# Kernel tuning notes

Hardware: AMD Instinct MI355X
Metric: run time of the kernel (lower is better)

The kernel has to match this reference:

```python
import jax, jax.numpy as jnp
import numpy as np

N_NODES = 100000
N_EDGES = 1600000
IN_CH = 128
OUT_CH = 128


def setup_inputs() -> dict:
    key = jax.random.key(0)
    k1, k2, k3 = jax.random.split(key, 3)
    x = jax.random.normal(k1, (N_NODES, IN_CH), dtype=jnp.float32)
    edge_index = jax.random.randint(k2, (2, N_EDGES), 0, N_NODES, dtype=jnp.int64)
    # Glorot-style init like PyG GCNConv
    W = jax.random.normal(k3, (IN_CH, OUT_CH), dtype=jnp.float32) * (1.0 / np.sqrt(IN_CH))
    b = jnp.zeros((OUT_CH,), dtype=jnp.float32)
    return {"x": x, "edge_index": edge_index, "W": W, "b": b}


def reference(x, edge_index, W, b):
    N = x.shape[0]
    # add self-loops (PyG GCNConv default add_self_loops=True)
    loop = jnp.arange(N, dtype=edge_index.dtype)
    src = jnp.concatenate([edge_index[0], loop])
    dst = jnp.concatenate([edge_index[1], loop])
    # symmetric normalization: deg computed over destination (col)
    deg = jax.ops.segment_sum(jnp.ones_like(src, dtype=x.dtype), dst, num_segments=N)
    dinv = jnp.where(deg > 0, jax.lax.rsqrt(deg), 0.0)
    norm = dinv[src] * dinv[dst]  # [E+N]
    xw = x @ W  # [N, out_ch]
    msg = xw[src] * norm[:, None]  # gather + scale, [E+N, out_ch]
    out = jax.ops.segment_sum(msg, dst, num_segments=N) + b  # scatter-add
    return jax.nn.relu(out)
```

## Files before the change

### kernel.cpp

```cpp
#include <hip/hip_runtime.h>
#include <hip/hip_bf16.h>

constexpr int CH    = 128;
constexpr int BSH   = 7;
constexpr int CAPSH = 12;
constexpr int CHUNK = 3125;
constexpr int CHCAP = 3200;
constexpr int BKCAP = 2816;

typedef __attribute__((ext_vector_type(8))) short short8v;
typedef __attribute__((ext_vector_type(4))) float f32x4;

__device__ __forceinline__ unsigned short f2bf(float f) {
    unsigned u = __float_as_uint(f);
    u = (u + 0x7fffu + ((u >> 16) & 1u)) >> 16;
    return (unsigned short)u;
}

__global__ __launch_bounds__(256) void k_bin(const int* __restrict__ src,
                                             const int* __restrict__ dst, int E,
                                             int* __restrict__ bucket_cnt,
                                             unsigned* __restrict__ packed,
                                             const float* __restrict__ W,
                                             unsigned short* __restrict__ Wt) {
    __shared__ int hist[1024];
    __shared__ int start[1024];
    __shared__ int cursor[1024];
    __shared__ int gofs[1024];
    __shared__ int tscan[256];
    __shared__ unsigned       sorted[CHCAP];
    __shared__ unsigned short sbkt[CHCAP];

    int t = threadIdx.x;
    if (blockIdx.x < 32) {
        int idx = blockIdx.x * 256 + t;
        int c  = idx & 127;
        int k2 = (idx >> 7) * 2;
        unsigned pk = (unsigned)f2bf(W[(size_t)k2 * CH + c]) |
                      ((unsigned)f2bf(W[(size_t)(k2 + 1) * CH + c]) << 16);
        *(unsigned*)(Wt + (size_t)c * CH + k2) = pk;
    }
    #pragma unroll
    for (int i = 0; i < 4; ++i) hist[t + i * 256] = 0;
    __syncthreads();

    int e0 = blockIdx.x * CHUNK;
    int e1 = min(e0 + CHUNK, E);
    for (int e = e0 + t; e < e1; e += 256)
        atomicAdd(&hist[dst[e] >> BSH], 1);
    __syncthreads();
    int b4 = t * 4;
    int c0 = hist[b4], c1 = hist[b4 + 1], c2 = hist[b4 + 2], c3 = hist[b4 + 3];
    int tsum = c0 + c1 + c2 + c3;
    tscan[t] = tsum;
    __syncthreads();
    for (int off = 1; off < 256; off <<= 1) {
        int v = (t >= off) ? tscan[t - off] : 0;
        __syncthreads();
        tscan[t] += v;
        __syncthreads();
    }
    int eb = tscan[t] - tsum;
    start[b4]     = eb;
    start[b4 + 1] = eb + c0;
    start[b4 + 2] = eb + c0 + c1;
    start[b4 + 3] = eb + c0 + c1 + c2;
    cursor[b4]     = eb;
    cursor[b4 + 1] = eb + c0;
    cursor[b4 + 2] = eb + c0 + c1;
    cursor[b4 + 3] = eb + c0 + c1 + c2;
    __syncthreads();
    #pragma unroll
    for (int i = 0; i < 4; ++i) {
        int b = t + i * 256;
        int c = hist[b];
        gofs[b] = (c > 0) ? atomicAdd(&bucket_cnt[b], c) : 0;
    }
    __syncthreads();
    for (int e = e0 + t; e < e1; e += 256) {
        int d = dst[e];
        int b = d >> BSH;
        int pos = atomicAdd(&cursor[b], 1);
        sorted[pos] = (unsigned)src[e] | ((unsigned)(d & ((1 << BSH) - 1)) << 20);
        sbkt[pos] = (unsigned short)b;
    }
    __syncthreads();
    int nloc = e1 - e0;
    for (int i = t; i < nloc; i += 256) {
        int b = sbkt[i];
        int gpos = (b << CAPSH) + gofs[b] + (i - start[b]);
        packed[gpos] = sorted[i];
    }
}

__global__ __launch_bounds__(256) void k_deg(const int* __restrict__ bucket_cnt,
                                             const unsigned* __restrict__ packed,
                                             float* __restrict__ dinv, int N) {
    __shared__ int fh[128];
    int b = blockIdx.x;
    int t = threadIdx.x;
    int cnt = bucket_cnt[b];
    if (t < 128) fh[t] = 0;
    __syncthreads();
    const unsigned* pk = packed + ((size_t)b << CAPSH);
    for (int i = t; i < cnt; i += 256)
        atomicAdd(&fh[(pk[i] >> 20) & 127], 1);
    __syncthreads();
    if (t < 128) {
        int node = (b << BSH) + t;
        if (node < N) dinv[node] = rsqrtf((float)fh[t] + 1.0f);
    }
}

__global__ __launch_bounds__(256) void k_gemm(const float* __restrict__ x,
                                              const unsigned short* __restrict__ Wt,
                                              const float* __restrict__ dinv,
                                              unsigned short* __restrict__ xwb, int N) {
    __shared__ __align__(16) unsigned short xs[64 * CH];
    int t = threadIdx.x;
    int w = t >> 6, lane = t & 63;
    int c16 = lane & 15, kq = lane >> 4, kb = kq * 8;
    int row0 = blockIdx.x * 64;
    int arow = row0 + w * 16 + c16;
    bool av = arow < N;
    const float* xp = x + (size_t)(av ? arow : 0) * CH;

    f32x4 acc[8];
    #pragma unroll
    for (int f = 0; f < 8; ++f) acc[f] = (f32x4){0.f, 0.f, 0.f, 0.f};

    #pragma unroll
    for (int kc = 0; kc < 4; ++kc) {
        float4 x0 = make_float4(0.f, 0.f, 0.f, 0.f), x1 = x0;
        if (av) {
            x0 = ((const float4*)(xp + kc * 32 + kb))[0];
            x1 = ((const float4*)(xp + kc * 32 + kb))[1];
        }
        union { short8v v; __hip_bfloat162 h[4]; } au;
        au.h[0] = __float22bfloat162_rn(make_float2(x0.x, x0.y));
        au.h[1] = __float22bfloat162_rn(make_float2(x0.z, x0.w));
        au.h[2] = __float22bfloat162_rn(make_float2(x1.x, x1.y));
        au.h[3] = __float22bfloat162_rn(make_float2(x1.z, x1.w));
        #pragma unroll
        for (int f = 0; f < 8; ++f) {
            short8v b = *(const short8v*)(Wt + (size_t)(f * 16 + c16) * CH + kc * 32 + kb);
            acc[f] = __builtin_amdgcn_mfma_f32_16x16x32_bf16(au.v, b, acc[f], 0, 0, 0);
        }
    }

    #pragma unroll
    for (int r = 0; r < 4; ++r) {
        int row_l = w * 16 + kq * 4 + r;
        int grow  = row0 + row_l;
        float dv  = (grow < N) ? dinv[grow] : 0.f;
        #pragma unroll
        for (int f = 0; f < 8; ++f) {
            int col = f * 16 + c16;
            unsigned bo = ((unsigned)((row_l * CH + col) * 2)) ^ ((unsigned)(row_l & 7) << 4);
            *(unsigned short*)((char*)xs + bo) = f2bf(acc[f][r] * dv);
        }
    }
    __syncthreads();
    #pragma unroll
    for (int i = 0; i < 4; ++i) {
        int g = i * 256 + t;
        int row_l = g >> 4;
        unsigned bo = ((unsigned)(g * 16)) ^ ((unsigned)(row_l & 7) << 4);
        uint4 v = *(const uint4*)((const char*)xs + bo);
        int row = row0 + row_l;
        if (row < N) ((uint4*)(xwb + (size_t)row * CH))[g & 15] = v;
    }
}

#define ACC8(U) \
    acc[0] += __uint_as_float((U).x << 16); \
    acc[1] += __uint_as_float((U).x & 0xffff0000u); \
    acc[2] += __uint_as_float((U).y << 16); \
    acc[3] += __uint_as_float((U).y & 0xffff0000u); \
    acc[4] += __uint_as_float((U).z << 16); \
    acc[5] += __uint_as_float((U).z & 0xffff0000u); \
    acc[6] += __uint_as_float((U).w << 16); \
    acc[7] += __uint_as_float((U).w & 0xffff0000u);

__global__ __launch_bounds__(512) void k_gather(const int* __restrict__ bucket_cnt,
                                                const unsigned* __restrict__ packed,
                                                const unsigned short* __restrict__ xwb,
                                                const float* __restrict__ dinv,
                                                const float* __restrict__ bias,
                                                float* __restrict__ out, int N) {
    __shared__ int fh[128];
    __shared__ int fs[128];
    __shared__ int fc[128];
    __shared__ unsigned spk[BKCAP];
    __shared__ int      elds[BKCAP];
    int b = blockIdx.x;
    int t = threadIdx.x;
    int cnt = min(bucket_cnt[b], BKCAP);
    const unsigned* pk = packed + ((size_t)b << CAPSH);

    if (t < 128) fh[t] = 0;
    __syncthreads();
    for (int i = t; i < cnt; i += 512) {
        unsigned p = pk[i];
        spk[i] = p;
        atomicAdd(&fh[(p >> 20) & 127], 1);
    }
    __syncthreads();
    if (t < 128) fs[t] = fh[t];
    __syncthreads();
    for (int off = 1; off < 128; off <<= 1) {
        int v = 0;
        if (t < 128 && t >= off) v = fs[t - off];
        __syncthreads();
        if (t < 128) fs[t] += v;
        __syncthreads();
    }
    if (t < 128) fc[t] = fs[t] - fh[t];
    __syncthreads();
    for (int i = t; i < cnt; i += 512) {
        unsigned p = spk[i];
        int f = (p >> 20) & 127;
        int pos = atomicAdd(&fc[f], 1);
        elds[pos] = (int)(p & 0xFFFFF);
    }
    __syncthreads();

    int wv = t >> 6, lane = t & 63;
    int q = lane >> 4, c16 = lane & 15;
    const uint4* xw4 = (const uint4*)xwb;
    for (int i = 0; i < 16; ++i) {
        int nl = wv * 16 + i;
        int n  = (b << BSH) + nl;
        if (n >= N) break;
        int deg = fh[nl];
        int beg = fs[nl] - deg;
        float acc[8];
        #pragma unroll
        for (int k = 0; k < 8; ++k) acc[k] = 0.f;

        for (int p0 = 0; p0 < deg; p0 += 64) {
            int m = deg - p0; if (m > 64) m = 64;
            int myi = 0;
            if (lane < m) myi = elds[beg + p0 + lane];
            int jj = q;
            int a  = __shfl(myi, jj);
            int s  = (jj < m) ? a : N;
            uint4 u = xw4[(size_t)s * 16 + c16];
            for (int j = 4; j < m; j += 4) {
                int jj2 = j + q;
                int ss  = __shfl(myi, jj2 & 63);
                int s2  = (jj2 < m) ? ss : N;
                uint4 u2 = xw4[(size_t)s2 * 16 + c16];
                ACC8(u);
                u = u2;
            }
            ACC8(u);
        }
        #pragma unroll
        for (int k = 0; k < 8; ++k) {
            acc[k] += __shfl_xor(acc[k], 16);
            acc[k] += __shfl_xor(acc[k], 32);
        }
        if (lane < 16) {
            float dn = dinv[n];
            uint4 u = xw4[(size_t)n * 16 + c16];
            ACC8(u);
            float4 b0 = ((const float4*)bias)[c16 * 2];
            float4 b1 = ((const float4*)bias)[c16 * 2 + 1];
            float4 o0, o1;
            o0.x = fmaxf(fmaf(acc[0], dn, b0.x), 0.f);
            o0.y = fmaxf(fmaf(acc[1], dn, b0.y), 0.f);
            o0.z = fmaxf(fmaf(acc[2], dn, b0.z), 0.f);
            o0.w = fmaxf(fmaf(acc[3], dn, b0.w), 0.f);
            o1.x = fmaxf(fmaf(acc[4], dn, b1.x), 0.f);
            o1.y = fmaxf(fmaf(acc[5], dn, b1.y), 0.f);
            o1.z = fmaxf(fmaf(acc[6], dn, b1.z), 0.f);
            o1.w = fmaxf(fmaf(acc[7], dn, b1.w), 0.f);
            ((float4*)(out + (size_t)n * CH))[c16 * 2]     = o0;
            ((float4*)(out + (size_t)n * CH))[c16 * 2 + 1] = o1;
        }
    }
}

extern "C" void kernel_launch(void* const* d_in, const int* in_sizes, int n_in,
                              void* d_out, int out_size, void* d_ws, size_t ws_size,
                              hipStream_t stream) {
    const float* x  = (const float*)d_in[0];
    const int*   ei = (const int*)d_in[1];
    const float* W  = (const float*)d_in[2];
    const float* b  = (const float*)d_in[3];

    int N = in_sizes[0] / CH;
    int E = in_sizes[1] / 2;
    const int* src = ei;
    const int* dst = ei + E;
    float* out = (float*)d_out;

    int nbuck = (N + (1 << BSH) - 1) >> BSH;
    size_t nslots = (size_t)nbuck << CAPSH;

    auto al = [](uintptr_t p) { return (p + 255) & ~(uintptr_t)255; };
    uintptr_t base = (uintptr_t)d_ws;
    unsigned short* xwb = (unsigned short*)base;
    int* bucket_cnt = (int*)(xwb + (size_t)(N + 1) * CH);
    uintptr_t p = al((uintptr_t)(bucket_cnt + nbuck));
    float* dinv     = (float*)p;               p = al(p + (size_t)N * 4);
    unsigned short* Wt = (unsigned short*)p;   p = al(p + (size_t)CH * CH * 2);
    unsigned* packed   = (unsigned*)p;

    int nbin = (E + CHUNK - 1) / CHUNK;

    hipMemsetAsync(xwb + (size_t)N * CH, 0, (size_t)CH * 2 + (size_t)nbuck * 4, stream);
    k_bin   <<<nbin, 256, 0, stream>>>(src, dst, E, bucket_cnt, packed, W, Wt);
    k_deg   <<<nbuck, 256, 0, stream>>>(bucket_cnt, packed, dinv, N);
    k_gemm  <<<(N + 63) / 64, 256, 0, stream>>>(x, Wt, dinv, xwb, N);
    k_gather<<<nbuck, 512, 0, stream>>>(bucket_cnt, packed, xwb, dinv, b, out, N);
}
```

Before: 150.8 us.

## Fold degree counting into binning via global atomics and drop k_deg kernel

Removes the separate degree kernel: k_bin now does a global atomicAdd per edge into a per-node degree array. The GEMM and gather kernels compute rsqrt(deg+1) inline instead of reading a dinv array. The gather kernel also drops its shared-memory staging copy of the packed edges and reads them twice from global, which lowers LDS use. The trade-off is 1.6M scattered global atomics in k_bin, which may cost more than the launch and pass they replace.

```diff
diff --git a/kernel.cpp b/kernel.cpp
--- a/kernel.cpp
+++ b/kernel.cpp
@@ -20,6 +20,7 @@
 __global__ __launch_bounds__(256) void k_bin(const int* __restrict__ src,
                                              const int* __restrict__ dst, int E,
                                              int* __restrict__ bucket_cnt,
+                                             int* __restrict__ deg,
                                              unsigned* __restrict__ packed,
                                              const float* __restrict__ W,
                                              unsigned short* __restrict__ Wt) {
@@ -83,6 +84,7 @@
         int pos = atomicAdd(&cursor[b], 1);
         sorted[pos] = (unsigned)src[e] | ((unsigned)(d & ((1 << BSH) - 1)) << 20);
         sbkt[pos] = (unsigned short)b;
+        atomicAdd(&deg[d], 1);
     }
     __syncthreads();
     int nloc = e1 - e0;
@@ -93,28 +95,9 @@
     }
 }
 
-__global__ __launch_bounds__(256) void k_deg(const int* __restrict__ bucket_cnt,
-                                             const unsigned* __restrict__ packed,
-                                             float* __restrict__ dinv, int N) {
-    __shared__ int fh[128];
-    int b = blockIdx.x;
-    int t = threadIdx.x;
-    int cnt = bucket_cnt[b];
-    if (t < 128) fh[t] = 0;
-    __syncthreads();
-    const unsigned* pk = packed + ((size_t)b << CAPSH);
-    for (int i = t; i < cnt; i += 256)
-        atomicAdd(&fh[(pk[i] >> 20) & 127], 1);
-    __syncthreads();
-    if (t < 128) {
-        int node = (b << BSH) + t;
-        if (node < N) dinv[node] = rsqrtf((float)fh[t] + 1.0f);
-    }
-}
-
 __global__ __launch_bounds__(256) void k_gemm(const float* __restrict__ x,
                                               const unsigned short* __restrict__ Wt,
-                                              const float* __restrict__ dinv,
+                                              const int* __restrict__ deg,
                                               unsigned short* __restrict__ xwb, int N) {
     __shared__ __align__(16) unsigned short xs[64 * CH];
     int t = threadIdx.x;
@@ -152,7 +135,7 @@
     for (int r = 0; r < 4; ++r) {
         int row_l = w * 16 + kq * 4 + r;
         int grow  = row0 + row_l;
-        float dv  = (grow < N) ? dinv[grow] : 0.f;
+        float dv  = (grow < N) ? rsqrtf((float)deg[grow] + 1.0f) : 0.f;
         #pragma unroll
         for (int f = 0; f < 8; ++f) {
             int col = f * 16 + c16;
@@ -185,14 +168,12 @@
 __global__ __launch_bounds__(512) void k_gather(const int* __restrict__ bucket_cnt,
                                                 const unsigned* __restrict__ packed,
                                                 const unsigned short* __restrict__ xwb,
-                                                const float* __restrict__ dinv,
                                                 const float* __restrict__ bias,
                                                 float* __restrict__ out, int N) {
     __shared__ int fh[128];
     __shared__ int fs[128];
     __shared__ int fc[128];
-    __shared__ unsigned spk[BKCAP];
-    __shared__ int      elds[BKCAP];
+    __shared__ int elds[BKCAP];
     int b = blockIdx.x;
     int t = threadIdx.x;
     int cnt = min(bucket_cnt[b], BKCAP);
@@ -200,11 +181,8 @@
 
     if (t < 128) fh[t] = 0;
     __syncthreads();
-    for (int i = t; i < cnt; i += 512) {
-        unsigned p = pk[i];
-        spk[i] = p;
-        atomicAdd(&fh[(p >> 20) & 127], 1);
-    }
+    for (int i = t; i < cnt; i += 512)
+        atomicAdd(&fh[(pk[i] >> 20) & 127], 1);
     __syncthreads();
     if (t < 128) fs[t] = fh[t];
     __syncthreads();
@@ -218,7 +196,7 @@
     if (t < 128) fc[t] = fs[t] - fh[t];
     __syncthreads();
     for (int i = t; i < cnt; i += 512) {
-        unsigned p = spk[i];
+        unsigned p = pk[i];
         int f = (p >> 20) & 127;
         int pos = atomicAdd(&fc[f], 1);
         elds[pos] = (int)(p & 0xFFFFF);
@@ -262,7 +240,7 @@
             acc[k] += __shfl_xor(acc[k], 32);
         }
         if (lane < 16) {
-            float dn = dinv[n];
+            float dn = rsqrtf((float)deg + 1.0f);
             uint4 u = xw4[(size_t)n * 16 + c16];
             ACC8(u);
             float4 b0 = ((const float4*)bias)[c16 * 2];
@@ -303,16 +281,16 @@
     uintptr_t base = (uintptr_t)d_ws;
     unsigned short* xwb = (unsigned short*)base;
     int* bucket_cnt = (int*)(xwb + (size_t)(N + 1) * CH);
-    uintptr_t p = al((uintptr_t)(bucket_cnt + nbuck));
-    float* dinv     = (float*)p;               p = al(p + (size_t)N * 4);
+    int* deg        = bucket_cnt + nbuck;
+    uintptr_t p = al((uintptr_t)(deg + N));
     unsigned short* Wt = (unsigned short*)p;   p = al(p + (size_t)CH * CH * 2);
     unsigned* packed   = (unsigned*)p;
 
     int nbin = (E + CHUNK - 1) / CHUNK;
 
-    hipMemsetAsync(xwb + (size_t)N * CH, 0, (size_t)CH * 2 + (size_t)nbuck * 4, stream);
-    k_bin   <<<nbin, 256, 0, stream>>>(src, dst, E, bucket_cnt, packed, W, Wt);
-    k_deg   <<<nbuck, 256, 0, stream>>>(bucket_cnt, packed, dinv, N);
-    k_gemm  <<<(N + 63) / 64, 256, 0, stream>>>(x, Wt, dinv, xwb, N);
-    k_gather<<<nbuck, 512, 0, stream>>>(bucket_cnt, packed, xwb, dinv, b, out, N);
-}
+    hipMemsetAsync(xwb + (size_t)N * CH, 0,
+                   (size_t)CH * 2 + (size_t)(nbuck + N) * 4, stream);
+    k_bin   <<<nbin, 256, 0, stream>>>(src, dst, E, bucket_cnt, deg, packed, W, Wt);
+    k_gemm  <<<(N + 63) / 64, 256, 0, stream>>>(x, Wt, deg, xwb, N);
+    k_gather<<<nbuck, 512, 0, stream>>>(bucket_cnt, packed, xwb, b, out, N);
+}
```

Result: slower. 204.3 us (+35.4%).
